# Performance work log

Measured on AMD Instinct MI355X. Metric: run time of the kernel, lower is better.

The kernel has to match this reference:

```python
import jax, jax.numpy as jnp
import numpy as np

M_DIM, Z_DIM, C = 256, 128, 32
N, L = 512, 384


def setup_inputs() -> dict:
    key = jax.random.key(0)
    ks = jax.random.split(key, 9)
    s = 1.0 / np.sqrt(M_DIM)
    return {
        "m": jax.random.normal(ks[0], (N, L, M_DIM), dtype=jnp.float32),
        "ln_gamma": jnp.ones((M_DIM,), jnp.float32),
        "ln_beta": jnp.zeros((M_DIM,), jnp.float32),
        "w1": jax.random.normal(ks[1], (M_DIM, C), jnp.float32) * s,
        "b1": jnp.zeros((C,), jnp.float32),
        "w2": jax.random.normal(ks[2], (M_DIM, C), jnp.float32) * s,
        "b2": jnp.zeros((C,), jnp.float32),
        "w3": jax.random.normal(ks[3], (C * C, Z_DIM), jnp.float32) * (1.0 / np.sqrt(C * C)),
        "b3": jnp.zeros((Z_DIM,), jnp.float32),
    }


def _layernorm(x, gamma, beta, eps=1e-5):
    mu = jnp.mean(x, axis=-1, keepdims=True)
    var = jnp.mean(jnp.square(x - mu), axis=-1, keepdims=True)
    return (x - mu) * jax.lax.rsqrt(var + eps) * gamma + beta


def reference(m, ln_gamma, ln_beta, w1, b1, w2, b2, w3, b3):
    n = m.shape[0]
    o = _layernorm(m, ln_gamma, ln_beta)          # (N, L, D)
    a = o @ w2 + b2                                # (N, L, C)  linear2
    b = o @ w1 + b1                                # (N, L, C)  linear1
    # mean over N of outer products: reassociated as a single contraction over n
    op = jnp.einsum('nia,njb->ijab', a, b) / n     # (L, L, C, C)
    ll = op.shape[0]
    z = op.reshape(ll, ll, -1) @ w3 + b3           # (L, L, Z)
    return z
```

## Files before the change

### kernel.cpp

```cpp
#include <hip/hip_runtime.h>
#include <hip/hip_bf16.h>
#include <stdint.h>

#define L_DIM 384
#define MD    256
#define CC    32
#define ZD    128
#define NB    512
#define K2    1024
#define MROWS 12288

typedef __attribute__((ext_vector_type(4)))  float f32x4;
typedef __attribute__((ext_vector_type(8)))  short bf16x8;

typedef __attribute__((address_space(1))) unsigned char* gcp;
typedef __attribute__((address_space(3))) unsigned char* lcp;

#define SBAR()  __builtin_amdgcn_s_barrier()
#define LGKM0() asm volatile("s_waitcnt lgkmcnt(0)" ::: "memory")
#define VMW(n)  asm volatile("s_waitcnt vmcnt(" #n ")" ::: "memory")
#define PRIO1() __builtin_amdgcn_s_setprio(1)
#define PRIO0() __builtin_amdgcn_s_setprio(0)

__device__ __forceinline__ unsigned short f2bf(float x) {
    union { float f; unsigned u; } v; v.f = x;
    unsigned r = v.u + 0x7fffu + ((v.u >> 16) & 1u);
    return (unsigned short)(r >> 16);
}

__device__ __forceinline__ uint2 pack4(unsigned short a, unsigned short b,
                                       unsigned short c, unsigned short d) {
    uint2 r; r.x = (unsigned)a | ((unsigned)b << 16);
    r.y = (unsigned)c | ((unsigned)d << 16); return r;
}

__global__ __launch_bounds__(256) void prep_kernel(
    const float* __restrict__ w1, const float* __restrict__ w2,
    const float* __restrict__ w3,
    unsigned short* __restrict__ w3frag, unsigned short* __restrict__ wfrag)
{
    int idx = blockIdx.x * 256 + threadIdx.x;
    if (idx < 131072) {
        int e = idx & 7, lane = (idx >> 3) & 63, zg = (idx >> 9) & 7, ks = idx >> 12;
        int k2p = ks * 32 + ((lane >> 4) << 3) + e;
        int wrow = (k2p & 31) * 32 + (k2p >> 5);
        int z  = zg * 16 + (lane & 15);
        w3frag[idx] = f2bf(w3[(size_t)wrow * ZD + z]);
    } else {
        int j = idx - 131072;
        int e = j & 7, lane = (j >> 3) & 63, nf = (j >> 9) & 3, ks = j >> 11;
        int c = nf * 16 + (lane & 15);
        int d = ks * 32 + ((lane >> 4) << 3) + e;
        float v = (c < CC) ? w2[d * CC + c] : w1[d * CC + (c - CC)];
        wfrag[j] = f2bf(v);
    }
}

__global__ __launch_bounds__(256, 4) void ln_proj_kernel(
    const float* __restrict__ mm, const float* __restrict__ gamma, const float* __restrict__ beta,
    const unsigned short* __restrict__ wfrag,
    const float* __restrict__ b1, const float* __restrict__ b2,
    unsigned short* __restrict__ At, unsigned short* __restrict__ Bt)
{
    __shared__ alignas(16) char o_b[32768];

    const int tid = threadIdx.x, wv = tid >> 6, lane = tid & 63;
    const int l0 = blockIdx.y * 2;
    const int n0 = blockIdx.x * 32;

    const int l_loc = wv >> 1;
    const int nbase = (wv & 1) << 4;
    const int l_g = l0 + l_loc;
    f32x4 g4 = *(const f32x4*)(gamma + lane * 4);
    f32x4 e4 = *(const f32x4*)(beta + lane * 4);

    #pragma unroll 4
    for (int r = 0; r < 16; ++r) {
        int row_loc = wv * 16 + r;
        int n_g = n0 + nbase + r;
        const float* src = mm + ((size_t)n_g * L_DIM + l_g) * MD + lane * 4;
        f32x4 x = *(const f32x4*)src;
        float s  = x[0] + x[1] + x[2] + x[3];
        float s2 = x[0]*x[0] + x[1]*x[1] + x[2]*x[2] + x[3]*x[3];
        #pragma unroll
        for (int off = 32; off > 0; off >>= 1) {
            s  += __shfl_xor(s,  off);
            s2 += __shfl_xor(s2, off);
        }
        float mu  = s * (1.0f / MD);
        float var = s2 * (1.0f / MD) - mu * mu;
        float rs  = rsqrtf(var + 1e-5f);
        unsigned short o0 = f2bf((x[0] - mu) * rs * g4[0] + e4[0]);
        unsigned short o1 = f2bf((x[1] - mu) * rs * g4[1] + e4[1]);
        unsigned short o2 = f2bf((x[2] - mu) * rs * g4[2] + e4[2]);
        unsigned short o3 = f2bf((x[3] - mu) * rs * g4[3] + e4[3]);
        *(uint2*)(o_b + row_loc * 512 + ((lane * 8) ^ ((row_loc & 7) << 4))) = pack4(o0, o1, o2, o3);
    }

    f32x4 acc[4] = {{0,0,0,0},{0,0,0,0},{0,0,0,0},{0,0,0,0}};
    const int lrow = lane & 15;
    const int kq16 = (lane >> 4) << 4;
    const int arow = wv * 16 + lrow;
    #pragma unroll
    for (int ks = 0; ks < 8; ++ks) {
        bf16x8 a = *(const bf16x8*)(o_b + arow * 512 + ((ks * 64 + kq16) ^ ((arow & 7) << 4)));
        #pragma unroll
        for (int nf = 0; nf < 4; ++nf) {
            bf16x8 b = *(const bf16x8*)(wfrag + (size_t)((ks * 4 + nf) * 64 + lane) * 8);
            acc[nf] = __builtin_amdgcn_mfma_f32_16x16x32_bf16(a, b, acc[nf], 0, 0, 0);
        }
    }

    const int rr0 = wv * 16 + ((lane >> 4) << 2);
    const int n_gw = n0 + (rr0 & 31);
    const int l_gw = l0 + (rr0 >> 5);
    #pragma unroll
    for (int nf = 0; nf < 4; ++nf) {
        int c = nf * 16 + lrow;
        float bias = (c < CC) ? b2[c] : b1[c - CC];
        uint2 pk = pack4(f2bf(acc[nf][0] + bias), f2bf(acc[nf][1] + bias),
                         f2bf(acc[nf][2] + bias), f2bf(acc[nf][3] + bias));
        if (c < CC) {
            *(uint2*)(At + (size_t)(l_gw * CC + c) * NB + n_gw) = pk;
        } else {
            int c31 = c - CC;
            int f = l_gw * 2 + (c31 >> 4);
            int lanep = (c31 & 15) + (((n_gw >> 3) & 3) << 4);
            size_t addr = ((size_t)(f * 16 + (n_gw >> 5)) * 64 + lanep) * 8 + (n_gw & 7);
            *(uint2*)(Bt + addr) = pk;
        }
    }
}

__global__ __launch_bounds__(512, 2) void opm_kernel(
    const unsigned short* __restrict__ At, const unsigned short* __restrict__ Bt,
    const unsigned short* __restrict__ w3frag, const float* __restrict__ b3,
    float* __restrict__ Z)
{
    __shared__ alignas(128) char smem[131072];
    char* const Ab = smem;

    const int tid = threadIdx.x, wv = tid >> 6, lane = tid & 63;

    const int lin = blockIdx.x;
    const int xcd = lin & 7, chunk = lin >> 3;
    const int i0 = (xcd * 6 + (chunk % 6)) * 256;
    const int j0 = (chunk / 6) * 256;

    const int lrow = lane & 15;
    const int kq16 = (lane >> 4) << 4;
    const int wr = (wv >> 2) * 128, wc = (wv & 3) * 64;

    const int srow = lane >> 3;
    const int spre = ((lane & 7) ^ srow) << 3;

    auto stageA = [&](int t) {
        char* base = Ab + (t & 1) * 32768;
        #pragma unroll
        for (int g = 0; g < 4; ++g) {
            int rl0 = g * 64 + wv * 8;
            const unsigned short* gp = At + (size_t)(i0 + rl0 + srow) * NB + t * 64 + spre;
            __builtin_amdgcn_global_load_lds((gcp)gp, (lcp)(base + rl0 * 128), 16, 0, 0);
        }
    };

    const int fb0 = (j0 + wc) >> 4;
    auto loadB = [&](bf16x8* bv, int t) {
        #pragma unroll
        for (int nf = 0; nf < 4; ++nf)
            #pragma unroll
            for (int kk = 0; kk < 2; ++kk)
                bv[nf * 2 + kk] = *(const bf16x8*)(Bt +
                    (size_t)((fb0 + nf) * 16 + (t * 2 + kk)) * 512 + lane * 8);
    };

    f32x4 acc[8][4] = {};
    bf16x8 bcur[8], bnxt[8], av[8];

    stageA(0); loadB(bcur, 0); stageA(1);
    VMW(12);
    SBAR();

    #pragma unroll
    for (int t = 0; t < 8; ++t) {
        if (t < 7) { stageA(t + 1); loadB(bnxt, t + 1); }
        const char* ab = Ab + (t & 1) * 32768;
        #pragma unroll
        for (int kk = 0; kk < 2; ++kk) {
            #pragma unroll
            for (int mf = 0; mf < 8; ++mf) {
                int row = wr + mf * 16 + lrow;
                av[mf] = *(const bf16x8*)(ab + row * 128 + ((kk * 64 + kq16) ^ ((row & 7) << 4)));
            }
            LGKM0();
            PRIO1();
            #pragma unroll
            for (int mf = 0; mf < 8; ++mf)
                #pragma unroll
                for (int nf = 0; nf < 4; ++nf)
                    acc[mf][nf] = __builtin_amdgcn_mfma_f32_16x16x32_bf16(
                        av[mf], bcur[nf * 2 + kk], acc[mf][nf], 0, 0, 0);
            PRIO0();
        }
        #pragma unroll
        for (int q = 0; q < 8; ++q) bcur[q] = bnxt[q];
        if (t < 7) { VMW(8); SBAR(); }
    }
    __syncthreads();

    char* const opb = smem;
    const int pfb = (wv >> 2) * 2, zgb = (wv & 3) * 2;
    const int row0 = pfb * 16 + lrow, row1 = row0 + 16;
    const int lq = lane >> 4;

    auto ldW = [&](int ks, int zg) -> bf16x8 {
        return *(const bf16x8*)(w3frag + (size_t)((ks * 8 + zg) * 64 + lane) * 8);
    };
    auto ldP = [&](int row, int ks) -> bf16x8 {
        int g = ks * 4 + lq;
        int b = g >> 2, jj = g & 3;
        int inner = (b * 64 + jj * 16) ^ (((b >> 1) & 7) << 4) ^ ((row & 7) << 4);
        return *(const bf16x8*)(opb + row * 2048 + inner);
    };

    bf16x8 wA0 = ldW(0, zgb), wA1 = ldW(0, zgb + 1);
    bf16x8 wB0 = ldW(1, zgb), wB1 = ldW(1, zgb + 1);

    const float scale = 1.0f / (float)NB;
    #pragma unroll
    for (int mf = 0; mf < 8; ++mf) {
        #pragma unroll
        for (int nf = 0; nf < 4; ++nf) {
            int col = wc + nf * 16 + lrow;
            int bcol = col & 31;
            int row = wr + mf * 16 + ((lane >> 4) << 2);
            int pl = ((row >> 5) << 3) | (col >> 5);
            int a0e = row & 31;
            int inner = (bcol * 64 + a0e * 2) ^ (((bcol >> 1) & 7) << 4) ^ ((pl & 7) << 4);
            *(uint2*)(opb + pl * 2048 + inner) =
                pack4(f2bf(acc[mf][nf][0] * scale), f2bf(acc[mf][nf][1] * scale),
                      f2bf(acc[mf][nf][2] * scale), f2bf(acc[mf][nf][3] * scale));
        }
    }
    __syncthreads();

    f32x4 acc2[2][2] = {};
    bf16x8 pA0 = ldP(row0, 0), pA1 = ldP(row1, 0);
    bf16x8 pB0 = ldP(row0, 1), pB1 = ldP(row1, 1);
    for (int ks = 0; ks < 32; ks += 2) {
        bf16x8 wN0 = {}, wN1 = {}, pN0 = {}, pN1 = {};
        bf16x8 wM0 = {}, wM1 = {}, pM0 = {}, pM1 = {};
        if (ks + 2 < 32) {
            wN0 = ldW(ks + 2, zgb); wN1 = ldW(ks + 2, zgb + 1);
            pN0 = ldP(row0, ks + 2); pN1 = ldP(row1, ks + 2);
            wM0 = ldW(ks + 3, zgb); wM1 = ldW(ks + 3, zgb + 1);
            pM0 = ldP(row0, ks + 3); pM1 = ldP(row1, ks + 3);
        }
        PRIO1();
        acc2[0][0] = __builtin_amdgcn_mfma_f32_16x16x32_bf16(pA0, wA0, acc2[0][0], 0, 0, 0);
        acc2[0][1] = __builtin_amdgcn_mfma_f32_16x16x32_bf16(pA0, wA1, acc2[0][1], 0, 0, 0);
        acc2[1][0] = __builtin_amdgcn_mfma_f32_16x16x32_bf16(pA1, wA0, acc2[1][0], 0, 0, 0);
        acc2[1][1] = __builtin_amdgcn_mfma_f32_16x16x32_bf16(pA1, wA1, acc2[1][1], 0, 0, 0);
        acc2[0][0] = __builtin_amdgcn_mfma_f32_16x16x32_bf16(pB0, wB0, acc2[0][0], 0, 0, 0);
        acc2[0][1] = __builtin_amdgcn_mfma_f32_16x16x32_bf16(pB0, wB1, acc2[0][1], 0, 0, 0);
        acc2[1][0] = __builtin_amdgcn_mfma_f32_16x16x32_bf16(pB1, wB0, acc2[1][0], 0, 0, 0);
        acc2[1][1] = __builtin_amdgcn_mfma_f32_16x16x32_bf16(pB1, wB1, acc2[1][1], 0, 0, 0);
        PRIO0();
        wA0 = wN0; wA1 = wN1; pA0 = pN0; pA1 = pN1;
        wB0 = wM0; wB1 = wM1; pB0 = pM0; pB1 = pM1;
    }

    const int pq = (lane >> 4) << 2;
    #pragma unroll
    for (int p = 0; p < 2; ++p) {
        #pragma unroll
        for (int zi = 0; zi < 2; ++zi) {
            int zc = (zgb + zi) * 16 + lrow;
            float bias = b3[zc];
            #pragma unroll
            for (int rr = 0; rr < 4; ++rr) {
                int pl = (pfb + p) * 16 + pq + rr;
                int ii = (i0 >> 5) + (pl >> 3);
                int jj = (j0 >> 5) + (pl & 7);
                Z[((size_t)ii * L_DIM + jj) * ZD + zc] = acc2[p][zi][rr] + bias;
            }
        }
    }
}

extern "C" void kernel_launch(void* const* d_in, const int* in_sizes, int n_in,
                              void* d_out, int out_size, void* d_ws, size_t ws_size,
                              hipStream_t stream)
{
    const float* mm    = (const float*)d_in[0];
    const float* gamma = (const float*)d_in[1];
    const float* beta  = (const float*)d_in[2];
    const float* w1    = (const float*)d_in[3];
    const float* b1    = (const float*)d_in[4];
    const float* w2    = (const float*)d_in[5];
    const float* b2    = (const float*)d_in[6];
    const float* w3    = (const float*)d_in[7];
    const float* b3    = (const float*)d_in[8];

    unsigned short* At     = (unsigned short*)d_ws;
    unsigned short* Bt     = At + (size_t)MROWS * NB;
    unsigned short* w3frag = Bt + (size_t)MROWS * NB;
    unsigned short* wfrag  = w3frag + 131072;

    prep_kernel<<<576, 256, 0, stream>>>(w1, w2, w3, w3frag, wfrag);
    ln_proj_kernel<<<dim3(16, 192), 256, 0, stream>>>(mm, gamma, beta, wfrag, b1, b2, At, Bt);
    opm_kernel<<<2304, 512, 0, stream>>>(At, Bt, w3frag, b3, (float*)d_out);
}
```

Baseline: 256.5 us.

## Store A in MFMA fragment layout and load both operands directly from global

The producer kernel now writes the A operand in the same pre-swizzled MFMA fragment layout as B. The main GEMM loop then drops LDS staging, the per-tile barriers and the waitcnt asm, and instead reads both A and B fragments straight from global memory into registers through a two-deep register double buffer. This removes LDS traffic and block-wide synchronization from the K loop. In exchange, each wave issues more global loads, A fragments are re-read across waves sharing rows instead of being shared in LDS, and register pressure rises.

```diff
diff --git a/kernel.cpp b/kernel.cpp
--- a/kernel.cpp
+++ b/kernel.cpp
@@ -13,12 +13,7 @@
 typedef __attribute__((ext_vector_type(4)))  float f32x4;
 typedef __attribute__((ext_vector_type(8)))  short bf16x8;
 
-typedef __attribute__((address_space(1))) unsigned char* gcp;
-typedef __attribute__((address_space(3))) unsigned char* lcp;
-
 #define SBAR()  __builtin_amdgcn_s_barrier()
-#define LGKM0() asm volatile("s_waitcnt lgkmcnt(0)" ::: "memory")
-#define VMW(n)  asm volatile("s_waitcnt vmcnt(" #n ")" ::: "memory")
 #define PRIO1() __builtin_amdgcn_s_setprio(1)
 #define PRIO0() __builtin_amdgcn_s_setprio(0)
 
@@ -120,25 +115,20 @@
         float bias = (c < CC) ? b2[c] : b1[c - CC];
         uint2 pk = pack4(f2bf(acc[nf][0] + bias), f2bf(acc[nf][1] + bias),
                          f2bf(acc[nf][2] + bias), f2bf(acc[nf][3] + bias));
-        if (c < CC) {
-            *(uint2*)(At + (size_t)(l_gw * CC + c) * NB + n_gw) = pk;
-        } else {
-            int c31 = c - CC;
-            int f = l_gw * 2 + (c31 >> 4);
-            int lanep = (c31 & 15) + (((n_gw >> 3) & 3) << 4);
-            size_t addr = ((size_t)(f * 16 + (n_gw >> 5)) * 64 + lanep) * 8 + (n_gw & 7);
-            *(uint2*)(Bt + addr) = pk;
-        }
+        int c31 = c & 31;
+        int f = l_gw * 2 + (c31 >> 4);
+        int lanep = (c31 & 15) + (((n_gw >> 3) & 3) << 4);
+        size_t addr = ((size_t)(f * 16 + (n_gw >> 5)) * 64 + lanep) * 8 + (n_gw & 7);
+        *(uint2*)(((c < CC) ? At : Bt) + addr) = pk;
     }
 }
 
 __global__ __launch_bounds__(512, 2) void opm_kernel(
-    const unsigned short* __restrict__ At, const unsigned short* __restrict__ Bt,
+    const unsigned short* __restrict__ Atf, const unsigned short* __restrict__ Btf,
     const unsigned short* __restrict__ w3frag, const float* __restrict__ b3,
     float* __restrict__ Z)
 {
     __shared__ alignas(128) char smem[131072];
-    char* const Ab = smem;
 
     const int tid = threadIdx.x, wv = tid >> 6, lane = tid & 63;
 
@@ -148,65 +138,42 @@
     const int j0 = (chunk / 6) * 256;
 
     const int lrow = lane & 15;
-    const int kq16 = (lane >> 4) << 4;
     const int wr = (wv >> 2) * 128, wc = (wv & 3) * 64;
-
-    const int srow = lane >> 3;
-    const int spre = ((lane & 7) ^ srow) << 3;
-
-    auto stageA = [&](int t) {
-        char* base = Ab + (t & 1) * 32768;
-        #pragma unroll
-        for (int g = 0; g < 4; ++g) {
-            int rl0 = g * 64 + wv * 8;
-            const unsigned short* gp = At + (size_t)(i0 + rl0 + srow) * NB + t * 64 + spre;
-            __builtin_amdgcn_global_load_lds((gcp)gp, (lcp)(base + rl0 * 128), 16, 0, 0);
-        }
-    };
-
+    const int fa0 = (i0 + wr) >> 4;
     const int fb0 = (j0 + wc) >> 4;
-    auto loadB = [&](bf16x8* bv, int t) {
+
+    f32x4 acc[8][4] = {};
+    bf16x8 av0[8], bv0[4], av1[8], bv1[4];
+
+    auto loadSet = [&](bf16x8* av, bf16x8* bv, int s) {
+        #pragma unroll
+        for (int mf = 0; mf < 8; ++mf)
+            av[mf] = *(const bf16x8*)(Atf + (size_t)((fa0 + mf) * 16 + s) * 512 + lane * 8);
         #pragma unroll
         for (int nf = 0; nf < 4; ++nf)
+            bv[nf] = *(const bf16x8*)(Btf + (size_t)((fb0 + nf) * 16 + s) * 512 + lane * 8);
+    };
+    auto mmSet = [&](bf16x8* av, bf16x8* bv) {
+        PRIO1();
+        #pragma unroll
+        for (int mf = 0; mf < 8; ++mf)
             #pragma unroll
-            for (int kk = 0; kk < 2; ++kk)
-                bv[nf * 2 + kk] = *(const bf16x8*)(Bt +
-                    (size_t)((fb0 + nf) * 16 + (t * 2 + kk)) * 512 + lane * 8);
-    };
-
-    f32x4 acc[8][4] = {};
-    bf16x8 bcur[8], bnxt[8], av[8];
-
-    stageA(0); loadB(bcur, 0); stageA(1);
-    VMW(12);
-    SBAR();
-
-    #pragma unroll
-    for (int t = 0; t < 8; ++t) {
-        if (t < 7) { stageA(t + 1); loadB(bnxt, t + 1); }
-        const char* ab = Ab + (t & 1) * 32768;
-        #pragma unroll
-        for (int kk = 0; kk < 2; ++kk) {
-            #pragma unroll
-            for (int mf = 0; mf < 8; ++mf) {
-                int row = wr + mf * 16 + lrow;
-                av[mf] = *(const bf16x8*)(ab + row * 128 + ((kk * 64 + kq16) ^ ((row & 7) << 4)));
-            }
-            LGKM0();
-            PRIO1();
-            #pragma unroll
-            for (int mf = 0; mf < 8; ++mf)
-                #pragma unroll
-                for (int nf = 0; nf < 4; ++nf)
-                    acc[mf][nf] = __builtin_amdgcn_mfma_f32_16x16x32_bf16(
-                        av[mf], bcur[nf * 2 + kk], acc[mf][nf], 0, 0, 0);
-            PRIO0();
-        }
-        #pragma unroll
-        for (int q = 0; q < 8; ++q) bcur[q] = bnxt[q];
-        if (t < 7) { VMW(8); SBAR(); }
-    }
-    __syncthreads();
+            for (int nf = 0; nf < 4; ++nf)
+                acc[mf][nf] = __builtin_amdgcn_mfma_f32_16x16x32_bf16(
+                    av[mf], bv[nf], acc[mf][nf], 0, 0, 0);
+        PRIO0();
+    };
+
+    loadSet(av0, bv0, 0);
+    loadSet(av1, bv1, 1);
+
+    #pragma unroll
+    for (int s = 0; s < 16; ++s) {
+        bf16x8* av = (s & 1) ? av1 : av0;
+        bf16x8* bv = (s & 1) ? bv1 : bv0;
+        mmSet(av, bv);
+        if (s + 2 < 16) loadSet(av, bv, s + 2);
+    }
 
     char* const opb = smem;
     const int pfb = (wv >> 2) * 2, zgb = (wv & 3) * 2;
```

Result: no change. 251.9 us (-1.8%).
